# Performance work log

Measured on AMD Instinct MI355X. Metric: run time of the kernel, lower is better.

## Reference

```python
import jax, jax.numpy as jnp
import numpy as np

N = 262144      # number of tokens/nodes
E = 262144      # number of dependency edges (~1 per token)
D_IN = 128
D_OUT = 128
L = 32          # number of dependency labels
R = 2 + 2 * L   # 'self', 'root', L forward labels, L reversed labels
SELF = 0        # index of 'self' weight


def setup_inputs() -> dict:
    key = jax.random.key(0)
    k1, k2, k3, k4, k5 = jax.random.split(key, 5)
    x = jax.random.normal(k1, (N, D_IN), dtype=jnp.float32)
    dep_idx = jax.random.randint(k2, (E,), 0, N)
    gov_idx = jax.random.randint(k3, (E,), 0, N)
    # edges grouped by relation label: labels occupy weight slots [2, 2+L)
    rel_idx = 2 + jnp.repeat(jnp.arange(L), E // L)
    # stacked Linear params: W[r] is [in, out] (== torch weight.T), b[r] is [out]
    W = jax.random.normal(k4, (R, D_IN, D_OUT), dtype=jnp.float32) / np.sqrt(D_IN)
    b = jax.random.normal(k5, (R, D_OUT), dtype=jnp.float32) * 0.01
    return {"x": x, "W": W, "b": b, "dep_idx": dep_idx,
            "gov_idx": gov_idx, "rel_idx": rel_idx}


def reference(x, W, b, dep_idx, gov_idx, rel_idx):
    n = x.shape[0]
    e = dep_idx.shape[0]
    eg = e // L  # edges per relation group (rel_idx is grouped/sorted)

    Wf, bf = W[2:2 + L], b[2:2 + L]           # forward-relation weights
    Wr, br = W[2 + L:2 + 2 * L], b[2 + L:]    # reversed-relation weights

    # forward messages: governor -> dependent, per-relation grouped GEMM
    xg = x[gov_idx].reshape(L, eg, D_IN)                      # [L, eg, in]
    msg_f = jnp.einsum('rei,rio->reo', xg, Wf) + bf[:, None]  # [L, eg, out]
    agg_f = jax.ops.segment_sum(msg_f.reshape(e, D_OUT), dep_idx,
                                num_segments=n)

    # reversed messages: dependent -> governor
    xd = x[dep_idx].reshape(L, eg, D_IN)
    msg_r = jnp.einsum('rei,rio->reo', xd, Wr) + br[:, None]
    agg_r = jax.ops.segment_sum(msg_r.reshape(e, D_OUT), gov_idx,
                                num_segments=n)

    # self transform for every token
    self_t = x @ W[SELF] + b[SELF]

    return jax.nn.relu(self_t + agg_f + agg_r)
```

## Files before the change

kernel.cpp:

```cpp
#include <hip/hip_runtime.h>
#include <hip/hip_bf16.h>
#include <stdint.h>

#define D_DIM 128
#define L_REL 32
#define MSG_LDW 132

typedef __attribute__((ext_vector_type(8))) short short8;
typedef __attribute__((ext_vector_type(4))) float f32x4;

__device__ __forceinline__ unsigned short f2bf(float f) {
    union { float f; unsigned u; } v; v.f = f;
    unsigned r = v.u + 0x7FFFu + ((v.u >> 16) & 1u);
    return (unsigned short)(r >> 16);
}
__device__ __forceinline__ float bf_lo(unsigned m) { return __uint_as_float(m << 16); }
__device__ __forceinline__ float bf_hi(unsigned m) { return __uint_as_float(m & 0xffff0000u); }

__device__ __forceinline__ void load_wfrag(const float* __restrict__ Wr,
                                           int w, int l15, int lq,
                                           short8 wf[2][4]) {
#pragma unroll
    for (int n = 0; n < 2; ++n) {
        int c = (w * 2 + n) * 16 + l15;
#pragma unroll
        for (int kk = 0; kk < 4; ++kk) {
            int kb = kk * 32 + lq * 8;
            short8 f;
#pragma unroll
            for (int j = 0; j < 8; ++j)
                f[j] = (short)f2bf(Wr[(size_t)(kb + j) * D_DIM + c]);
            wf[n][kk] = f;
        }
    }
}

__device__ __forceinline__ void mfma_tile(const unsigned short* xs,
                                          const short8 wf[2][4],
                                          int l15, int lq, f32x4 acc[4][2]) {
#pragma unroll
    for (int kk = 0; kk < 4; ++kk) {
        short8 a[4];
#pragma unroll
        for (int m = 0; m < 4; ++m) {
            int row = m * 16 + l15;
            unsigned byte = ((unsigned)(row * 256 + (kk * 32 + lq * 8) * 2))
                          ^ (((unsigned)(row & 7)) << 4);
            a[m] = *reinterpret_cast<const short8*>(
                       reinterpret_cast<const char*>(xs) + byte);
        }
#pragma unroll
        for (int m = 0; m < 4; ++m)
#pragma unroll
            for (int n = 0; n < 2; ++n)
                acc[m][n] = __builtin_amdgcn_mfma_f32_16x16x32_bf16(
                                a[m], wf[n][kk], acc[m][n], 0, 0, 0);
    }
}

__global__ void hist_kernel(const int* __restrict__ dep, const int* __restrict__ gov,
                            int* __restrict__ deg, int E) {
    int i = blockIdx.x * blockDim.x + threadIdx.x;
    int stride = gridDim.x * blockDim.x;
    for (; i < E; i += stride) {
        atomicAdd(&deg[dep[i]], 1);
        atomicAdd(&deg[gov[i]], 1);
    }
}

__global__ __launch_bounds__(256) void scanA_kernel(const int* __restrict__ deg,
                                                    int* __restrict__ off,
                                                    int* __restrict__ partials) {
    __shared__ int ls[256];
    const int tid = threadIdx.x;
    const int gi = blockIdx.x * 256 + tid;
    int4 v = ((const int4*)deg)[gi];
    int s = v.x + v.y + v.z + v.w;
    ls[tid] = s;
    __syncthreads();
    for (int o = 1; o < 256; o <<= 1) {
        int t = (tid >= o) ? ls[tid - o] : 0;
        __syncthreads();
        ls[tid] += t;
        __syncthreads();
    }
    int e0 = ls[tid] - s;
    int4 e; e.x = e0; e.y = e0 + v.x; e.z = e.y + v.y; e.w = e.z + v.z;
    ((int4*)off)[gi] = e;
    if (tid == 255) partials[blockIdx.x] = ls[255];
}

__global__ __launch_bounds__(256) void scanB_kernel(int* __restrict__ partials) {
    __shared__ int ls[256];
    const int tid = threadIdx.x;
    int v = partials[tid];
    ls[tid] = v;
    __syncthreads();
    for (int o = 1; o < 256; o <<= 1) {
        int t = (tid >= o) ? ls[tid - o] : 0;
        __syncthreads();
        ls[tid] += t;
        __syncthreads();
    }
    partials[tid] = ls[tid] - v;
}

__global__ __launch_bounds__(256) void scanC_kernel(int* __restrict__ off,
                                                    int* __restrict__ cur,
                                                    const int* __restrict__ partials) {
    const int p = partials[blockIdx.x];
    const int gi = blockIdx.x * 256 + threadIdx.x;
    int4 v = ((int4*)off)[gi];
    v.x += p; v.y += p; v.z += p; v.w += p;
    ((int4*)off)[gi] = v;
    ((int4*)cur)[gi] = v;
}

#define CPB 4
__global__ __launch_bounds__(256) void msg_kernel(const float* __restrict__ x,
                                                  const float* __restrict__ W,
                                                  const float* __restrict__ b,
                                                  const int* __restrict__ dep,
                                                  const int* __restrict__ gov,
                                                  int* __restrict__ cur,
                                                  unsigned* __restrict__ msg,
                                                  int eg, int blocksPerRel) {
    __shared__ __align__(16) char smem[64 * MSG_LDW * 2];
    unsigned short* xs = (unsigned short*)smem;
    unsigned short* tr = (unsigned short*)smem;
    __shared__ int sidx[CPB][64];
    __shared__ int didx[CPB][64];
    __shared__ int pos[64];

    const int tid = threadIdx.x;
    const int lane = tid & 63, w = tid >> 6;
    const int l15 = lane & 15, lq = lane >> 4;

    const int bid = blockIdx.x;
    const int vr = bid / blocksPerRel;
    const int blk = bid % blocksPerRel;
    const int r = vr & 31;
    const bool fwd = (vr < 32);
    const int* __restrict__ srcI = fwd ? gov : dep;
    const int* __restrict__ dstI = fwd ? dep : gov;

    const int ebase0 = r * eg + blk * CPB * 64;
    {
        int c = tid >> 6, t = tid & 63;
        sidx[c][t] = srcI[ebase0 + c * 64 + t];
        didx[c][t] = dstI[ebase0 + c * 64 + t];
    }

    short8 wf[2][4];
    load_wfrag(W + (size_t)(2 + vr) * D_DIM * D_DIM, w, l15, lq, wf);
    float bias[2];
#pragma unroll
    for (int n = 0; n < 2; ++n)
        bias[n] = b[(size_t)(2 + vr) * D_DIM + (w * 2 + n) * 16 + l15];

    __syncthreads();

    for (int ch = 0; ch < CPB; ++ch) {
#pragma unroll
        for (int it = 0; it < 8; ++it) {
            int flat = it * 256 + tid;
            int row = flat >> 5, f4 = flat & 31;
            float4 v = *reinterpret_cast<const float4*>(
                           x + (size_t)sidx[ch][row] * D_DIM + f4 * 4);
            unsigned lo = (unsigned)f2bf(v.x) | ((unsigned)f2bf(v.y) << 16);
            unsigned hi = (unsigned)f2bf(v.z) | ((unsigned)f2bf(v.w) << 16);
            unsigned byte = ((unsigned)(row * 256 + f4 * 8))
                          ^ (((unsigned)(row & 7)) << 4);
            *reinterpret_cast<uint2*>(reinterpret_cast<char*>(xs) + byte) =
                make_uint2(lo, hi);
        }
        __syncthreads();

        f32x4 acc[4][2];
#pragma unroll
        for (int m = 0; m < 4; ++m)
#pragma unroll
            for (int n = 0; n < 2; ++n) acc[m][n] = (f32x4){0.f, 0.f, 0.f, 0.f};
        mfma_tile(xs, wf, l15, lq, acc);

        if (tid < 64) pos[tid] = atomicAdd(&cur[didx[ch][tid]], 1);
        __syncthreads();

#pragma unroll
        for (int m = 0; m < 4; ++m)
#pragma unroll
            for (int reg = 0; reg < 4; ++reg) {
                int row = m * 16 + lq * 4 + reg;
#pragma unroll
                for (int n = 0; n < 2; ++n)
                    tr[row * MSG_LDW + w * 32 + n * 16 + l15] =
                        f2bf(acc[m][n][reg] + bias[n]);
            }
        __syncthreads();

#pragma unroll
        for (int i = 0; i < 16; ++i) {
            int r0 = w * 16 + i;
            unsigned dw = *reinterpret_cast<const unsigned*>(
                              reinterpret_cast<const char*>(tr)
                              + r0 * MSG_LDW * 2 + lane * 4);
            msg[(size_t)pos[r0] * 64 + lane] = dw;
        }
        __syncthreads();
    }
}

__global__ __launch_bounds__(256) void agg_kernel(const float* __restrict__ x,
                                                  const float* __restrict__ W,
                                                  const float* __restrict__ b,
                                                  const int* __restrict__ off,
                                                  const int* __restrict__ deg,
                                                  const unsigned* __restrict__ msg,
                                                  float* __restrict__ out) {
    __shared__ __align__(16) char smem[64 * MSG_LDW * 2];
    unsigned short* xs = (unsigned short*)smem;
    unsigned short* st = (unsigned short*)smem;
    __shared__ int offs[64 + 1];

    const int tid = threadIdx.x;
    const int lane = tid & 63, w = tid >> 6;
    const int l15 = lane & 15, lq = lane >> 4;
    const int base = blockIdx.x * 64;

    if (tid < 64) offs[tid] = off[base + tid];
    if (tid == 64) offs[64] = off[base + 63] + deg[base + 63];

    short8 wf[2][4];
    load_wfrag(W, w, l15, lq, wf);
    float bias[2];
#pragma unroll
    for (int n = 0; n < 2; ++n) bias[n] = b[(w * 2 + n) * 16 + l15];

#pragma unroll
    for (int it = 0; it < 8; ++it) {
        int flat = it * 256 + tid;
        int row = flat >> 5, f4 = flat & 31;
        float4 v = *reinterpret_cast<const float4*>(
                       x + (size_t)(base + row) * D_DIM + f4 * 4);
        unsigned lo = (unsigned)f2bf(v.x) | ((unsigned)f2bf(v.y) << 16);
        unsigned hi = (unsigned)f2bf(v.z) | ((unsigned)f2bf(v.w) << 16);
        unsigned byte = ((unsigned)(row * 256 + f4 * 8))
                      ^ (((unsigned)(row & 7)) << 4);
        *reinterpret_cast<uint2*>(reinterpret_cast<char*>(xs) + byte) =
            make_uint2(lo, hi);
    }
    __syncthreads();

    f32x4 acc[4][2];
#pragma unroll
    for (int m = 0; m < 4; ++m)
#pragma unroll
        for (int n = 0; n < 2; ++n) acc[m][n] = (f32x4){0.f, 0.f, 0.f, 0.f};
    mfma_tile(xs, wf, l15, lq, acc);
    __syncthreads();

#pragma unroll
    for (int m = 0; m < 4; ++m)
#pragma unroll
        for (int reg = 0; reg < 4; ++reg) {
            int row = m * 16 + lq * 4 + reg;
#pragma unroll
            for (int n = 0; n < 2; ++n)
                st[row * MSG_LDW + w * 32 + n * 16 + l15] =
                    f2bf(acc[m][n][reg] + bias[n]);
        }
    __syncthreads();

    const int nfirst = w * 16;
    int ci = 0;
    float2 accm = make_float2(0.f, 0.f);

#define FLUSH_NODE()                                                          \
    do {                                                                      \
        const unsigned sv = *reinterpret_cast<const unsigned*>(               \
            reinterpret_cast<const char*>(st)                                 \
            + (nfirst + ci) * MSG_LDW * 2 + lane * 4);                        \
        float2 so;                                                            \
        so.x = fmaxf(bf_lo(sv) + accm.x, 0.f);                                \
        so.y = fmaxf(bf_hi(sv) + accm.y, 0.f);                                \
        *reinterpret_cast<float2*>(                                           \
            out + (size_t)(base + nfirst + ci) * D_DIM + lane * 2) = so;      \
        accm.x = 0.f; accm.y = 0.f;                                           \
        ++ci;                                                                 \
    } while (0)

    const int s0 = offs[nfirst];
    const int s1 = offs[nfirst + 16];
    int nb = offs[nfirst + 1];
    int j = s0;
    const unsigned* mp = msg + (size_t)j * 64 + lane;

    for (; j + 8 <= s1; j += 8, mp += 512) {
        unsigned v[8];
#pragma unroll
        for (int k = 0; k < 8; ++k) v[k] = mp[k * 64];
#pragma unroll
        for (int k = 0; k < 8; ++k) {
            int jj = j + k;
            while (jj >= nb) { FLUSH_NODE(); nb = offs[nfirst + ci + 1]; }
            accm.x += bf_lo(v[k]); accm.y += bf_hi(v[k]);
        }
    }
    for (; j < s1; ++j, mp += 64) {
        unsigned v = mp[0];
        while (j >= nb) { FLUSH_NODE(); nb = offs[nfirst + ci + 1]; }
        accm.x += bf_lo(v); accm.y += bf_hi(v);
    }
    while (ci < 16) FLUSH_NODE();
#undef FLUSH_NODE
}

__global__ __launch_bounds__(256) void self_kernel(const float* __restrict__ x,
                                                   const float* __restrict__ W,
                                                   const float* __restrict__ b,
                                                   float* __restrict__ out) {
    __shared__ unsigned short xs[64 * D_DIM];
    const int tid = threadIdx.x;
    const int lane = tid & 63, w = tid >> 6;
    const int l15 = lane & 15, lq = lane >> 4;
    short8 wf[2][4];
    load_wfrag(W, w, l15, lq, wf);
    float bias[2];
#pragma unroll
    for (int n = 0; n < 2; ++n) bias[n] = b[(w * 2 + n) * 16 + l15];
    const int rbase = blockIdx.x * 64;
#pragma unroll
    for (int it = 0; it < 8; ++it) {
        int flat = it * 256 + tid;
        int row = flat >> 5, f4 = flat & 31;
        float4 v = *reinterpret_cast<const float4*>(
                       x + (size_t)(rbase + row) * D_DIM + f4 * 4);
        unsigned lo = (unsigned)f2bf(v.x) | ((unsigned)f2bf(v.y) << 16);
        unsigned hi = (unsigned)f2bf(v.z) | ((unsigned)f2bf(v.w) << 16);
        unsigned byte = ((unsigned)(row * 256 + f4 * 8))
                      ^ (((unsigned)(row & 7)) << 4);
        *reinterpret_cast<uint2*>(reinterpret_cast<char*>(xs) + byte) =
            make_uint2(lo, hi);
    }
    __syncthreads();
    f32x4 acc[4][2];
#pragma unroll
    for (int m = 0; m < 4; ++m)
#pragma unroll
        for (int n = 0; n < 2; ++n) acc[m][n] = (f32x4){0.f, 0.f, 0.f, 0.f};
    mfma_tile(xs, wf, l15, lq, acc);
#pragma unroll
    for (int m = 0; m < 4; ++m)
#pragma unroll
        for (int reg = 0; reg < 4; ++reg) {
            int row = rbase + m * 16 + lq * 4 + reg;
#pragma unroll
            for (int n = 0; n < 2; ++n) {
                int c = (w * 2 + n) * 16 + l15;
                out[(size_t)row * D_DIM + c] = acc[m][n][reg] + bias[n];
            }
        }
}

__global__ __launch_bounds__(256) void edge_kernel(const float* __restrict__ x,
                                                   const float* __restrict__ W,
                                                   const float* __restrict__ b,
                                                   const int* __restrict__ dep,
                                                   const int* __restrict__ gov,
                                                   float* __restrict__ out,
                                                   int eg, int blocksPerRel) {
    __shared__ unsigned short xs[64 * D_DIM];
    __shared__ int sidx[CPB][64];
    __shared__ int didx[CPB][64];
    const int tid = threadIdx.x;
    const int lane = tid & 63, w = tid >> 6;
    const int l15 = lane & 15, lq = lane >> 4;
    const int bid = blockIdx.x;
    const int vr = bid / blocksPerRel;
    const int blk = bid % blocksPerRel;
    const int r = vr & 31;
    const bool fwd = (vr < 32);
    const int* __restrict__ srcI = fwd ? gov : dep;
    const int* __restrict__ dstI = fwd ? dep : gov;
    const int ebase0 = r * eg + blk * CPB * 64;
    {
        int c = tid >> 6, t = tid & 63;
        sidx[c][t] = srcI[ebase0 + c * 64 + t];
        didx[c][t] = dstI[ebase0 + c * 64 + t];
    }
    short8 wf[2][4];
    load_wfrag(W + (size_t)(2 + vr) * D_DIM * D_DIM, w, l15, lq, wf);
    float bias[2];
#pragma unroll
    for (int n = 0; n < 2; ++n)
        bias[n] = b[(size_t)(2 + vr) * D_DIM + (w * 2 + n) * 16 + l15];
    __syncthreads();
#pragma unroll
    for (int ch = 0; ch < CPB; ++ch) {
#pragma unroll
        for (int it = 0; it < 8; ++it) {
            int flat = it * 256 + tid;
            int row = flat >> 5, f4 = flat & 31;
            float4 v = *reinterpret_cast<const float4*>(
                           x + (size_t)sidx[ch][row] * D_DIM + f4 * 4);
            unsigned lo = (unsigned)f2bf(v.x) | ((unsigned)f2bf(v.y) << 16);
            unsigned hi = (unsigned)f2bf(v.z) | ((unsigned)f2bf(v.w) << 16);
            unsigned byte = ((unsigned)(row * 256 + f4 * 8))
                          ^ (((unsigned)(row & 7)) << 4);
            *reinterpret_cast<uint2*>(reinterpret_cast<char*>(xs) + byte) =
                make_uint2(lo, hi);
        }
        __syncthreads();
        f32x4 acc[4][2];
#pragma unroll
        for (int m = 0; m < 4; ++m)
#pragma unroll
            for (int n = 0; n < 2; ++n) acc[m][n] = (f32x4){0.f, 0.f, 0.f, 0.f};
        mfma_tile(xs, wf, l15, lq, acc);
#pragma unroll
        for (int m = 0; m < 4; ++m)
#pragma unroll
            for (int reg = 0; reg < 4; ++reg) {
                int erow = m * 16 + lq * 4 + reg;
                int dst = didx[ch][erow];
#pragma unroll
                for (int n = 0; n < 2; ++n) {
                    int c = (w * 2 + n) * 16 + l15;
                    unsafeAtomicAdd(&out[(size_t)dst * D_DIM + c],
                                    acc[m][n][reg] + bias[n]);
                }
            }
        __syncthreads();
    }
}

__global__ void relu_kernel(float* __restrict__ o, int n4) {
    int i = blockIdx.x * blockDim.x + threadIdx.x;
    int stride = gridDim.x * blockDim.x;
    float4* p = reinterpret_cast<float4*>(o);
    for (; i < n4; i += stride) {
        float4 v = p[i];
        v.x = fmaxf(v.x, 0.f); v.y = fmaxf(v.y, 0.f);
        v.z = fmaxf(v.z, 0.f); v.w = fmaxf(v.w, 0.f);
        p[i] = v;
    }
}

extern "C" void kernel_launch(void* const* d_in, const int* in_sizes, int n_in,
                              void* d_out, int out_size, void* d_ws, size_t ws_size,
                              hipStream_t stream) {
    const float* x   = (const float*)d_in[0];
    const float* W   = (const float*)d_in[1];
    const float* b   = (const float*)d_in[2];
    const int*   dep = (const int*)d_in[3];
    const int*   gov = (const int*)d_in[4];
    float* out = (float*)d_out;

    const int N  = in_sizes[0] / D_DIM;
    const int E  = in_sizes[3];
    const int eg = E / L_REL;

    const size_t msgBytes = (size_t)2 * E * 64 * sizeof(unsigned);
    const size_t need = msgBytes + (size_t)(3 * N + 256) * 4 + 4096;

    if (ws_size >= need) {
        char* basep = (char*)d_ws;
        unsigned* msg = (unsigned*)basep;
        int* deg = (int*)(basep + msgBytes);
        int* off = deg + (size_t)N;
        int* cur = off + (size_t)N;
        int* partials = cur + (size_t)N;

        hipMemsetAsync(deg, 0, (size_t)N * sizeof(int), stream);
        hist_kernel<<<512, 256, 0, stream>>>(dep, gov, deg, E);
        scanA_kernel<<<N / 1024, 256, 0, stream>>>(deg, off, partials);
        scanB_kernel<<<1, 256, 0, stream>>>(partials);
        scanC_kernel<<<N / 1024, 256, 0, stream>>>(off, cur, partials);

        const int blocksPerRel = eg / 64 / CPB;
        msg_kernel<<<64 * blocksPerRel, 256, 0, stream>>>(x, W, b, dep, gov,
                                                          cur, msg, eg,
                                                          blocksPerRel);
        agg_kernel<<<N / 64, 256, 0, stream>>>(x, W, b, off, deg, msg, out);
    } else {
        self_kernel<<<N / 64, 256, 0, stream>>>(x, W, b, out);
        const int blocksPerRel = eg / 64 / CPB;
        edge_kernel<<<64 * blocksPerRel, 256, 0, stream>>>(x, W, b, dep, gov, out,
                                                           eg, blocksPerRel);
        relu_kernel<<<2048, 256, 0, stream>>>(out, out_size / 4);
    }
}
```

Before: 212.6 us.

## Precompute bf16 copy of x and stage tiles via direct global-to-LDS loads

Adds a prep kernel that converts x to bf16 once into workspace, then the message and aggregation kernels gather bf16 rows straight into swizzled LDS using global_load_lds instead of loading fp32, converting and writing LDS per element. This halves the gathered bytes per edge (x is read about five times across the edge and self passes) and removes per-chunk conversion ALU and register traffic. It costs an extra full pass over x plus a bf16 buffer in workspace, and falls back to the old path when the workspace is too small.

```diff
diff --git a/kernel.cpp b/kernel.cpp
--- a/kernel.cpp
+++ b/kernel.cpp
@@ -16,6 +16,12 @@
 }
 __device__ __forceinline__ float bf_lo(unsigned m) { return __uint_as_float(m << 16); }
 __device__ __forceinline__ float bf_hi(unsigned m) { return __uint_as_float(m & 0xffff0000u); }
+
+__device__ __forceinline__ void gload16(const void* g, void* l) {
+    __builtin_amdgcn_global_load_lds(
+        (const __attribute__((address_space(1))) unsigned*)g,
+        (__attribute__((address_space(3))) unsigned*)l, 16, 0, 0);
+}
 
 __device__ __forceinline__ void load_wfrag(const float* __restrict__ Wr,
                                            int w, int l15, int lq,
@@ -55,6 +61,24 @@
             for (int n = 0; n < 2; ++n)
                 acc[m][n] = __builtin_amdgcn_mfma_f32_16x16x32_bf16(
                                 a[m], wf[n][kk], acc[m][n], 0, 0, 0);
+    }
+}
+
+__global__ __launch_bounds__(256) void prep_kernel(const float* __restrict__ x,
+                                                   uint4* __restrict__ xb,
+                                                   int n8) {
+    int i = blockIdx.x * blockDim.x + threadIdx.x;
+    int stride = gridDim.x * blockDim.x;
+    const float4* x4 = (const float4*)x;
+    for (; i < n8; i += stride) {
+        float4 a = x4[2 * i];
+        float4 c = x4[2 * i + 1];
+        uint4 o;
+        o.x = (unsigned)f2bf(a.x) | ((unsigned)f2bf(a.y) << 16);
+        o.y = (unsigned)f2bf(a.z) | ((unsigned)f2bf(a.w) << 16);
+        o.z = (unsigned)f2bf(c.x) | ((unsigned)f2bf(c.y) << 16);
+        o.w = (unsigned)f2bf(c.z) | ((unsigned)f2bf(c.w) << 16);
+        xb[i] = o;
     }
 }
 
@@ -117,7 +141,9 @@
 }
 
 #define CPB 4
+template <bool XB>
 __global__ __launch_bounds__(256) void msg_kernel(const float* __restrict__ x,
+                                                  const unsigned short* __restrict__ xb,
                                                   const float* __restrict__ W,
                                                   const float* __restrict__ b,
                                                   const int* __restrict__ dep,
@@ -161,18 +187,31 @@
     __syncthreads();
 
     for (int ch = 0; ch < CPB; ++ch) {
-#pragma unroll
-        for (int it = 0; it < 8; ++it) {
-            int flat = it * 256 + tid;
-            int row = flat >> 5, f4 = flat & 31;
-            float4 v = *reinterpret_cast<const float4*>(
-                           x + (size_t)sidx[ch][row] * D_DIM + f4 * 4);
-            unsigned lo = (unsigned)f2bf(v.x) | ((unsigned)f2bf(v.y) << 16);
-            unsigned hi = (unsigned)f2bf(v.z) | ((unsigned)f2bf(v.w) << 16);
-            unsigned byte = ((unsigned)(row * 256 + f4 * 8))
-                          ^ (((unsigned)(row & 7)) << 4);
-            *reinterpret_cast<uint2*>(reinterpret_cast<char*>(xs) + byte) =
-                make_uint2(lo, hi);
+        if constexpr (XB) {
+#pragma unroll
+            for (int i = 0; i < 4; ++i) {
+                const int rbase = w * 16 + i * 4;
+                const int row = rbase + (lane >> 4);
+                const int src = sidx[ch][row];
+                const unsigned off = ((unsigned)((lane & 15) * 16))
+                                   ^ (((unsigned)(row & 7)) << 4);
+                gload16((const char*)(xb + (size_t)src * D_DIM) + off,
+                        (char*)xs + rbase * 256);
+            }
+        } else {
+#pragma unroll
+            for (int it = 0; it < 8; ++it) {
+                int flat = it * 256 + tid;
+                int row = flat >> 5, f4 = flat & 31;
+                float4 v = *reinterpret_cast<const float4*>(
+                               x + (size_t)sidx[ch][row] * D_DIM + f4 * 4);
+                unsigned lo = (unsigned)f2bf(v.x) | ((unsigned)f2bf(v.y) << 16);
+                unsigned hi = (unsigned)f2bf(v.z) | ((unsigned)f2bf(v.w) << 16);
+                unsigned byte = ((unsigned)(row * 256 + f4 * 8))
+                              ^ (((unsigned)(row & 7)) << 4);
+                *reinterpret_cast<uint2*>(reinterpret_cast<char*>(xs) + byte) =
+                    make_uint2(lo, hi);
+            }
         }
         __syncthreads();
 
@@ -210,7 +249,9 @@
     }
 }
 
+template <bool XB>
 __global__ __launch_bounds__(256) void agg_kernel(const float* __restrict__ x,
+                                                  const unsigned short* __restrict__ xb,
                                                   const float* __restrict__ W,
                                                   const float* __restrict__ b,
                                                   const int* __restrict__ off,
@@ -236,18 +277,30 @@
 #pragma unroll
     for (int n = 0; n < 2; ++n) bias[n] = b[(w * 2 + n) * 16 + l15];
 
-#pragma unroll
-    for (int it = 0; it < 8; ++it) {
-        int flat = it * 256 + tid;
-        int row = flat >> 5, f4 = flat & 31;
-        float4 v = *reinterpret_cast<const float4*>(
-                       x + (size_t)(base + row) * D_DIM + f4 * 4);
-        unsigned lo = (unsigned)f2bf(v.x) | ((unsigned)f2bf(v.y) << 16);
-        unsigned hi = (unsigned)f2bf(v.z) | ((unsigned)f2bf(v.w) << 16);
-        unsigned byte = ((unsigned)(row * 256 + f4 * 8))
-                      ^ (((unsigned)(row & 7)) << 4);
-        *reinterpret_cast<uint2*>(reinterpret_cast<char*>(xs) + byte) =
-            make_uint2(lo, hi);
+    if constexpr (XB) {
+#pragma unroll
+        for (int i = 0; i < 4; ++i) {
+            const int rbase = w * 16 + i * 4;
+            const int row = rbase + (lane >> 4);
+            const unsigned off16 = ((unsigned)((lane & 15) * 16))
+                                 ^ (((unsigned)(row & 7)) << 4);
+            gload16((const char*)(xb + (size_t)(base + row) * D_DIM) + off16,
+                    (char*)xs + rbase * 256);
+        }
+    } else {
+#pragma unroll
+        for (int it = 0; it < 8; ++it) {
+            int flat = it * 256 + tid;
+            int row = flat >> 5, f4 = flat & 31;
+            float4 v = *reinterpret_cast<const float4*>(
+                           x + (size_t)(base + row) * D_DIM + f4 * 4);
+            unsigned lo = (unsigned)f2bf(v.x) | ((unsigned)f2bf(v.y) << 16);
+            unsigned hi = (unsigned)f2bf(v.z) | ((unsigned)f2bf(v.w) << 16);
+            unsigned byte = ((unsigned)(row * 256 + f4 * 8))
+                          ^ (((unsigned)(row & 7)) << 4);
+            *reinterpret_cast<uint2*>(reinterpret_cast<char*>(xs) + byte) =
+                make_uint2(lo, hi);
+        }
     }
     __syncthreads();
 
@@ -461,30 +514,47 @@
     const int eg = E / L_REL;
 
     const size_t msgBytes = (size_t)2 * E * 64 * sizeof(unsigned);
-    const size_t need = msgBytes + (size_t)(3 * N + 256) * 4 + 4096;
-
-    if (ws_size >= need) {
+    const size_t xbBytes  = (size_t)N * D_DIM * 2;
+    const size_t csrBytes = (size_t)(3 * N + 256) * 4;
+    const size_t needFull = msgBytes + xbBytes + csrBytes + 4096;
+    const size_t needMid  = msgBytes + csrBytes + 4096;
+
+    const int blocksPerRel = eg / 64 / CPB;
+
+    if (ws_size >= needMid) {
+        const bool full = (ws_size >= needFull);
         char* basep = (char*)d_ws;
         unsigned* msg = (unsigned*)basep;
-        int* deg = (int*)(basep + msgBytes);
+        char* p2 = basep + msgBytes;
+        unsigned short* xb = nullptr;
+        if (full) { xb = (unsigned short*)p2; p2 += xbBytes; }
+        int* deg = (int*)p2;
         int* off = deg + (size_t)N;
         int* cur = off + (size_t)N;
         int* partials = cur + (size_t)N;
 
         hipMemsetAsync(deg, 0, (size_t)N * sizeof(int), stream);
+        if (full)
+            prep_kernel<<<2048, 256, 0, stream>>>(x, (uint4*)xb,
+                                                  N * D_DIM / 8);
         hist_kernel<<<512, 256, 0, stream>>>(dep, gov, deg, E);
         scanA_kernel<<<N / 1024, 256, 0, stream>>>(deg, off, partials);
         scanB_kernel<<<1, 256, 0, stream>>>(partials);
         scanC_kernel<<<N / 1024, 256, 0, stream>>>(off, cur, partials);
 
-        const int blocksPerRel = eg / 64 / CPB;
-        msg_kernel<<<64 * blocksPerRel, 256, 0, stream>>>(x, W, b, dep, gov,
-                                                          cur, msg, eg,
-                                                          blocksPerRel);
-        agg_kernel<<<N / 64, 256, 0, stream>>>(x, W, b, off, deg, msg, out);
+        if (full) {
+            msg_kernel<true><<<64 * blocksPerRel, 256, 0, stream>>>(
+                x, xb, W, b, dep, gov, cur, msg, eg, blocksPerRel);
+            agg_kernel<true><<<N / 64, 256, 0, stream>>>(
+                x, xb, W, b, off, deg, msg, out);
+        } else {
+            msg_kernel<false><<<64 * blocksPerRel, 256, 0, stream>>>(
+                x, nullptr, W, b, dep, gov, cur, msg, eg, blocksPerRel);
+            agg_kernel<false><<<N / 64, 256, 0, stream>>>(
+                x, nullptr, W, b, off, deg, msg, out);
+        }
     } else {
         self_kernel<<<N / 64, 256, 0, stream>>>(x, W, b, out);
-        const int blocksPerRel = eg / 64 / CPB;
         edge_kernel<<<64 * blocksPerRel, 256, 0, stream>>>(x, W, b, dep, gov, out,
                                                            eg, blocksPerRel);
         relu_kernel<<<2048, 256, 0, stream>>>(out, out_size / 4);
```

After: 225.2 us. 1.06x slower.

## Prefetch next chunk's gathered rows in msg_kernel and deepen agg load unroll

Applied to the files above, without the earlier changes.

msg_kernel now gives the gather buffer and the transpose buffer separate shared-memory arrays. It issues the global loads for the next 64-edge chunk's source rows before the current chunk's MFMA, atomics and scatter stores, then converts them to bf16 and writes them into shared memory afterwards. This hides gather latency behind compute and drops one barrier per chunk. The cost is more shared memory and 32 extra VGPRs for the prefetch registers, which may lower occupancy. agg_kernel's message-load batch also grows from 8 to 16 outstanding loads per lane.

```diff
diff --git a/kernel.cpp b/kernel.cpp
--- a/kernel.cpp
+++ b/kernel.cpp
@@ -5,6 +5,7 @@
 #define D_DIM 128
 #define L_REL 32
 #define MSG_LDW 132
+#define CPB 4
 
 typedef __attribute__((ext_vector_type(8))) short short8;
 typedef __attribute__((ext_vector_type(4))) float f32x4;
@@ -116,7 +117,6 @@
     ((int4*)cur)[gi] = v;
 }
 
-#define CPB 4
 __global__ __launch_bounds__(256) void msg_kernel(const float* __restrict__ x,
                                                   const float* __restrict__ W,
                                                   const float* __restrict__ b,
@@ -125,9 +125,8 @@
                                                   int* __restrict__ cur,
                                                   unsigned* __restrict__ msg,
                                                   int eg, int blocksPerRel) {
-    __shared__ __align__(16) char smem[64 * MSG_LDW * 2];
-    unsigned short* xs = (unsigned short*)smem;
-    unsigned short* tr = (unsigned short*)smem;
+    __shared__ __align__(16) unsigned short xs[64 * 128];
+    __shared__ __align__(16) unsigned short tr[64 * MSG_LDW];
     __shared__ int sidx[CPB][64];
     __shared__ int didx[CPB][64];
     __shared__ int pos[64];
@@ -158,23 +157,39 @@
     for (int n = 0; n < 2; ++n)
         bias[n] = b[(size_t)(2 + vr) * D_DIM + (w * 2 + n) * 16 + l15];
 
+    const int srow = tid >> 5;
+    const int sf4  = tid & 31;
+    __syncthreads();
+
+    float4 st[8];
+#pragma unroll
+    for (int it = 0; it < 8; ++it) {
+        int row = it * 8 + srow;
+        st[it] = *reinterpret_cast<const float4*>(
+                     x + (size_t)sidx[0][row] * D_DIM + sf4 * 4);
+    }
+#pragma unroll
+    for (int it = 0; it < 8; ++it) {
+        int row = it * 8 + srow;
+        unsigned lo = (unsigned)f2bf(st[it].x) | ((unsigned)f2bf(st[it].y) << 16);
+        unsigned hi = (unsigned)f2bf(st[it].z) | ((unsigned)f2bf(st[it].w) << 16);
+        unsigned byte = ((unsigned)(row * 256 + sf4 * 8))
+                      ^ (((unsigned)(row & 7)) << 4);
+        *reinterpret_cast<uint2*>(reinterpret_cast<char*>(xs) + byte) =
+            make_uint2(lo, hi);
+    }
     __syncthreads();
 
     for (int ch = 0; ch < CPB; ++ch) {
-#pragma unroll
-        for (int it = 0; it < 8; ++it) {
-            int flat = it * 256 + tid;
-            int row = flat >> 5, f4 = flat & 31;
-            float4 v = *reinterpret_cast<const float4*>(
-                           x + (size_t)sidx[ch][row] * D_DIM + f4 * 4);
-            unsigned lo = (unsigned)f2bf(v.x) | ((unsigned)f2bf(v.y) << 16);
-            unsigned hi = (unsigned)f2bf(v.z) | ((unsigned)f2bf(v.w) << 16);
-            unsigned byte = ((unsigned)(row * 256 + f4 * 8))
-                          ^ (((unsigned)(row & 7)) << 4);
-            *reinterpret_cast<uint2*>(reinterpret_cast<char*>(xs) + byte) =
-                make_uint2(lo, hi);
-        }
-        __syncthreads();
+        float4 nx[8];
+        if (ch + 1 < CPB) {
+#pragma unroll
+            for (int it = 0; it < 8; ++it) {
+                int row = it * 8 + srow;
+                nx[it] = *reinterpret_cast<const float4*>(
+                             x + (size_t)sidx[ch + 1][row] * D_DIM + sf4 * 4);
+            }
+        }
 
         f32x4 acc[4][2];
 #pragma unroll
@@ -184,7 +199,6 @@
         mfma_tile(xs, wf, l15, lq, acc);
 
         if (tid < 64) pos[tid] = atomicAdd(&cur[didx[ch][tid]], 1);
-        __syncthreads();
 
 #pragma unroll
         for (int m = 0; m < 4; ++m)
@@ -206,7 +220,19 @@
                               + r0 * MSG_LDW * 2 + lane * 4);
             msg[(size_t)pos[r0] * 64 + lane] = dw;
         }
-        __syncthreads();
+        if (ch + 1 < CPB) {
+#pragma unroll
+            for (int it = 0; it < 8; ++it) {
+                int row = it * 8 + srow;
+                unsigned lo = (unsigned)f2bf(nx[it].x) | ((unsigned)f2bf(nx[it].y) << 16);
+                unsigned hi = (unsigned)f2bf(nx[it].z) | ((unsigned)f2bf(nx[it].w) << 16);
+                unsigned byte = ((unsigned)(row * 256 + sf4 * 8))
+                              ^ (((unsigned)(row & 7)) << 4);
+                *reinterpret_cast<uint2*>(reinterpret_cast<char*>(xs) + byte) =
+                    make_uint2(lo, hi);
+            }
+            __syncthreads();
+        }
     }
 }
 
@@ -295,12 +321,12 @@
     int j = s0;
     const unsigned* mp = msg + (size_t)j * 64 + lane;
 
-    for (; j + 8 <= s1; j += 8, mp += 512) {
-        unsigned v[8];
-#pragma unroll
-        for (int k = 0; k < 8; ++k) v[k] = mp[k * 64];
-#pragma unroll
-        for (int k = 0; k < 8; ++k) {
+    for (; j + 16 <= s1; j += 16, mp += 1024) {
+        unsigned v[16];
+#pragma unroll
+        for (int k = 0; k < 16; ++k) v[k] = mp[k * 64];
+#pragma unroll
+        for (int k = 0; k < 16; ++k) {
             int jj = j + k;
             while (jj >= nb) { FLUSH_NODE(); nb = offs[nfirst + ci + 1]; }
             accm.x += bf_lo(v[k]); accm.y += bf_hi(v[k]);
@@ -463,6 +489,8 @@
     const size_t msgBytes = (size_t)2 * E * 64 * sizeof(unsigned);
     const size_t need = msgBytes + (size_t)(3 * N + 256) * 4 + 4096;
 
+    const int blocksPerRel = eg / 64 / CPB;
+
     if (ws_size >= need) {
         char* basep = (char*)d_ws;
         unsigned* msg = (unsigned*)basep;
@@ -477,14 +505,12 @@
         scanB_kernel<<<1, 256, 0, stream>>>(partials);
         scanC_kernel<<<N / 1024, 256, 0, stream>>>(off, cur, partials);
 
-        const int blocksPerRel = eg / 64 / CPB;
         msg_kernel<<<64 * blocksPerRel, 256, 0, stream>>>(x, W, b, dep, gov,
                                                           cur, msg, eg,
                                                           blocksPerRel);
         agg_kernel<<<N / 64, 256, 0, stream>>>(x, W, b, off, deg, msg, out);
     } else {
         self_kernel<<<N / 64, 256, 0, stream>>>(x, W, b, out);
-        const int blocksPerRel = eg / 64 / CPB;
         edge_kernel<<<64 * blocksPerRel, 256, 0, stream>>>(x, W, b, dep, gov, out,
                                                            eg, blocksPerRel);
         relu_kernel<<<2048, 256, 0, stream>>>(out, out_size / 4);
```

Result: no change. 213.7 us (+0.5%).
